# Kernel optimization log

Measured on AMD Instinct MI355X. Metric: run time of the kernel, lower is better.

The kernel has to match this reference:

```python
import jax, jax.numpy as jnp
import numpy as np

IN_F = 4096
OUT_F = 4096
Q_RANK = 2
R_RANK = 2
SCALE = 1.0
B, S = 2, 2048


def setup_inputs() -> dict:
    key = jax.random.key(0)
    ks = jax.random.split(key, 8)
    inp = jax.random.normal(ks[0], (B, S, IN_F), jnp.float32)
    # Q, R come from a QR decomposition of linear.weight.t(); random stand-ins with
    # matching shapes and O(1) scale are fine for a numerical baseline.
    Q = jax.random.normal(ks[1], (IN_F, OUT_F), jnp.float32) / np.sqrt(IN_F).astype(np.float32)
    R = jax.random.normal(ks[2], (OUT_F, OUT_F), jnp.float32) / np.sqrt(OUT_F).astype(np.float32)
    # kron_Q1/Q2 are initialized to identity in __init__ (never re-initialized);
    # add small noise so the rotation path is non-trivial.
    sq1 = IN_F // Q_RANK
    kron_Q1 = jnp.eye(sq1, dtype=jnp.float32) + 0.01 * jax.random.normal(ks[3], (sq1, sq1), jnp.float32)
    kron_Q2 = jnp.eye(Q_RANK, dtype=jnp.float32) + 0.01 * jax.random.normal(ks[4], (Q_RANK, Q_RANK), jnp.float32)
    # kron_R1/R2 use normal init with std = 1/size.
    sr1 = OUT_F // R_RANK
    kron_R1 = jax.random.normal(ks[5], (sr1, sr1), jnp.float32) / sr1
    kron_R2 = jax.random.normal(ks[6], (R_RANK, R_RANK), jnp.float32) / R_RANK
    # lambda_matrix inits to zeros; use small noise so the delta term is exercised.
    lambda_matrix = 0.01 * jax.random.normal(ks[7], (OUT_F,), jnp.float32)
    return {"input": inp, "Q": Q, "R": R, "kron_Q1": kron_Q1, "kron_Q2": kron_Q2,
            "kron_R1": kron_R1, "kron_R2": kron_R2, "lambda_matrix": lambda_matrix}


def reference(input, Q, R, kron_Q1, kron_Q2, kron_R1, kron_R2, lambda_matrix):
    rotation = jnp.kron(kron_Q1, kron_Q2)          # [in, in]
    orth = jnp.kron(kron_R1, kron_R2)              # [out, out]
    # orth @ diag(lambda) @ orth.T without materializing diag
    R_eff = R + (orth * lambda_matrix[None, :]) @ orth.T  # [out, out]
    W_t = rotation @ (Q @ R_eff)                   # [in, out]
    # F.linear(input, W_t.t()) == input @ W_t; dropout is identity in eval; bias=False
    return (input @ W_t) * SCALE
```

## Files before the change

kernel.cpp:

```cpp
#include <hip/hip_runtime.h>
#include <stdint.h>


typedef unsigned short u16;
typedef short bf16x8 __attribute__((ext_vector_type(8)));
typedef float f32x4 __attribute__((ext_vector_type(4)));

__device__ __forceinline__ u16 f2bf(float f) {
  union { float f; uint32_t u; } v; v.f = f;
  return (u16)((v.u + 0x7FFFu + ((v.u >> 16) & 1u)) >> 16);
}

__device__ __forceinline__ void store_out(float* p, float v) { *p = v; }
__device__ __forceinline__ void store_out(u16* p, float v) { *p = f2bf(v); }

__device__ __forceinline__ void gload_lds16(const u16* g, u16* l) {
  __builtin_amdgcn_global_load_lds(
      (__attribute__((address_space(1))) void*)(uintptr_t)g,
      (__attribute__((address_space(3))) void*)l, 16, 0, 0);
}

template <typename OutT>
__global__ __launch_bounds__(512, 2) void gemm256(
    const u16* __restrict__ A, const u16* __restrict__ Bt, OutT* __restrict__ C,
    int M, int N, int K, int ldC, long long sA, long long sC) {
  extern __shared__ __align__(16) u16 smem[];
  u16* ldsA = smem;
  u16* ldsB = smem + 32768;

  const int tid  = (int)threadIdx.x;
  const int lane = tid & 63;
  const int wid  = tid >> 6;
  const int wr   = wid >> 2;
  const int wc   = wid & 3;

  const int tilesX = (int)gridDim.x;
  const int tilesXY = tilesX * (int)gridDim.y;
  const int nwg = tilesXY * (int)gridDim.z;
  const int bid = ((int)blockIdx.z * (int)gridDim.y + (int)blockIdx.y) * tilesX + (int)blockIdx.x;
  const int swz = (bid & 7) * (nwg >> 3) + (bid >> 3);
  const int z   = swz / tilesXY;
  const int rem = swz % tilesXY;
  const int brow = (rem / tilesX) << 8;
  const int bcol = (rem % tilesX) << 8;
  A += (size_t)z * sA;
  C += (size_t)z * sC;

  const int lr = lane & 15, lg = lane >> 4, h = lr >> 1;
  const int sf = (lg + ((lr & 1) << 2)) ^ h;
  const int aoff = (wr * 64 + h) * 64 + sf * 8;
  const int boff = (wc * 32 + h) * 64 + sf * 8;

  const int kp   = (tid & 7) ^ ((tid >> 3) & 7);
  const int srow = 2 * (tid >> 3) + (kp >> 2);
  const int scol = (kp & 3) << 3;
  const size_t gA0 = (size_t)(brow + srow) * K + scol;
  const size_t gA1 = (size_t)(brow + 128 + srow) * K + scol;
  const size_t gB0 = (size_t)(bcol + srow) * K + scol;
  const size_t gB1 = (size_t)(bcol + 128 + srow) * K + scol;
  const int sOff0 = wid * 512;
  const int sOff1 = 4096 + wid * 512;

  const int NC = K >> 5;

  f32x4 acc[8][4] = {};

#define STAGE_A(cc) do { const int _s = ((cc) & 3) * 8192; const size_t _k = (size_t)(cc) * 32; \
    gload_lds16(A + gA0 + _k, ldsA + _s + sOff0);                                               \
    gload_lds16(A + gA1 + _k, ldsA + _s + sOff1); } while (0)
#define STAGE_B(cc) do { const int _s = ((cc) & 3) * 8192; const size_t _k = (size_t)(cc) * 32; \
    gload_lds16(Bt + gB0 + _k, ldsB + _s + sOff0);                                              \
    gload_lds16(Bt + gB1 + _k, ldsB + _s + sOff1); } while (0)

  STAGE_A(0); STAGE_B(0); STAGE_A(1); STAGE_B(1); STAGE_A(2); STAGE_B(2);
  asm volatile("s_waitcnt vmcnt(8)" ::: "memory");
  __builtin_amdgcn_sched_barrier(0);
  __builtin_amdgcn_s_barrier();

#define CHUNK(c, DOSTAGE, TAILWAIT) do {                                        \
    const int _sl = ((c) & 3) * 8192;                                           \
    const u16* _pa = ldsA + _sl + aoff;                                         \
    const u16* _pb = ldsB + _sl + boff;                                         \
    bf16x8 aA[4], aB[4], bb[4];                                                 \
    _Pragma("unroll")                                                           \
    for (int m = 0; m < 4; ++m) aA[m] = *(const bf16x8*)(_pa + m * 512);        \
    _Pragma("unroll")                                                           \
    for (int n = 0; n < 4; ++n) bb[n] = *(const bf16x8*)(_pb + n * 512);        \
    if (DOSTAGE) STAGE_A((c) + 3);                                              \
    __builtin_amdgcn_s_barrier();                                               \
    asm volatile("s_waitcnt lgkmcnt(0)" ::: "memory");                          \
    __builtin_amdgcn_sched_barrier(0);                                          \
    __builtin_amdgcn_s_setprio(1);                                              \
    _Pragma("unroll")                                                           \
    for (int m = 0; m < 4; ++m)                                                 \
      _Pragma("unroll")                                                         \
      for (int n = 0; n < 4; ++n)                                               \
        acc[m][n] = __builtin_amdgcn_mfma_f32_16x16x32_bf16(aA[m], bb[n], acc[m][n], 0, 0, 0); \
    __builtin_amdgcn_s_setprio(0);                                              \
    __builtin_amdgcn_s_barrier();                                               \
    _Pragma("unroll")                                                           \
    for (int m = 0; m < 4; ++m) aB[m] = *(const bf16x8*)(_pa + (4 + m) * 512);  \
    if (DOSTAGE) STAGE_B((c) + 3);                                              \
    __builtin_amdgcn_s_barrier();                                               \
    asm volatile("s_waitcnt lgkmcnt(0)" ::: "memory");                          \
    __builtin_amdgcn_sched_barrier(0);                                          \
    __builtin_amdgcn_s_setprio(1);                                              \
    _Pragma("unroll")                                                           \
    for (int m = 0; m < 4; ++m)                                                 \
      _Pragma("unroll")                                                         \
      for (int n = 0; n < 4; ++n)                                               \
        acc[4 + m][n] = __builtin_amdgcn_mfma_f32_16x16x32_bf16(aB[m], bb[n], acc[4 + m][n], 0, 0, 0); \
    __builtin_amdgcn_s_setprio(0);                                              \
    asm volatile("s_waitcnt " TAILWAIT ::: "memory");                           \
    __builtin_amdgcn_sched_barrier(0);                                          \
    __builtin_amdgcn_s_barrier();                                               \
  } while (0)

  for (int c = 0; c + 3 < NC; ++c) CHUNK(c, 1, "vmcnt(8)");
  CHUNK(NC - 3, 0, "vmcnt(4)");
  CHUNK(NC - 2, 0, "vmcnt(0)");
  CHUNK(NC - 1, 0, "vmcnt(0)");

#undef CHUNK
#undef STAGE_A
#undef STAGE_B

#pragma unroll
  for (int m = 0; m < 8; ++m) {
    const int r0 = brow + wr * 128 + m * 16 + lg * 4;
#pragma unroll
    for (int n = 0; n < 4; ++n) {
      const int cc = bcol + wc * 64 + n * 16 + lr;
#pragma unroll
      for (int j = 0; j < 4; ++j)
        store_out(&C[(size_t)(r0 + j) * ldC + cc], acc[m][n][j]);
    }
  }
}

__global__ void trans_kernel(const float* __restrict__ in, u16* __restrict__ out, int n) {
  __shared__ float t[32][33];
  const int bx = (int)blockIdx.x * 32, by = (int)blockIdx.y * 32;
  const int x = (int)threadIdx.x, y0 = (int)threadIdx.y;
#pragma unroll
  for (int dy = 0; dy < 32; dy += 8)
    t[y0 + dy][x] = in[(size_t)(bx + y0 + dy) * n + by + x];
  __syncthreads();
#pragma unroll
  for (int dy = 0; dy < 32; dy += 8)
    out[(size_t)(by + y0 + dy) * n + bx + x] = f2bf(t[x][y0 + dy]);
}

__global__ void transperm_kernel(const float* __restrict__ in, u16* __restrict__ out) {
  __shared__ float t[32][33];
  const int bx = (int)blockIdx.x * 32, by = (int)blockIdx.y * 32;
  const int x = (int)threadIdx.x, y0 = (int)threadIdx.y;
#pragma unroll
  for (int dy = 0; dy < 32; dy += 8)
    t[y0 + dy][x] = in[(size_t)(bx + y0 + dy) * 4096 + by + x];
  __syncthreads();
  const int r = bx + x;
  const int cp = ((r & 1) << 11) | (r >> 1);
#pragma unroll
  for (int dy = 0; dy < 32; dy += 8)
    out[(size_t)(by + y0 + dy) * 4096 + cp] = f2bf(t[x][y0 + dy]);
}

__global__ void transadd_kernel(const float* __restrict__ R, const float* __restrict__ Dsub,
                                u16* __restrict__ out) {
  __shared__ float t[32][33];
  const int bx = (int)blockIdx.x * 32, by = (int)blockIdx.y * 32;
  const int x = (int)threadIdx.x, y0 = (int)threadIdx.y;
#pragma unroll
  for (int dy = 0; dy < 32; dy += 8)
    t[y0 + dy][x] = R[(size_t)(bx + y0 + dy) * 4096 + by + x];
  __syncthreads();
  const int j = bx + x;
#pragma unroll
  for (int dy = 0; dy < 32; dy += 8) {
    const int i = by + y0 + dy;
    const int s = ((i & 1) << 1) | (j & 1);
    const float d = Dsub[(size_t)s * 4194304 + ((size_t)(i >> 1) << 11) + (j >> 1)];
    out[(size_t)i * 4096 + j] = f2bf(t[x][y0 + dy] + d);
  }
}

__global__ void scale_r1_kernel(const float* __restrict__ R1, const float* __restrict__ R2,
                                const float* __restrict__ lam,
                                u16* __restrict__ R1bf, u16* __restrict__ Asc) {
  const int idx = (int)blockIdx.x * 256 + (int)threadIdx.x;
  const int i1 = idx >> 9, k1 = (idx & 511) << 2;
  const float4 r1 = *(const float4*)(R1 + (size_t)i1 * 2048 + k1);
  const float4 l0 = *(const float4*)(lam + 2 * k1);
  const float4 l1 = *(const float4*)(lam + 2 * k1 + 4);
  const float le[4] = {l0.x, l0.z, l1.x, l1.z};
  const float lo[4] = {l0.y, l0.w, l1.y, l1.w};
  const float rv[4] = {r1.x, r1.y, r1.z, r1.w};
  ushort4 rb;
  rb.x = f2bf(r1.x); rb.y = f2bf(r1.y); rb.z = f2bf(r1.z); rb.w = f2bf(r1.w);
  *(ushort4*)(R1bf + (size_t)i1 * 2048 + k1) = rb;
#pragma unroll
  for (int s = 0; s < 4; ++s) {
    const int i2 = s >> 1, j2 = s & 1;
    const float c0 = R2[i2 * 2] * R2[j2 * 2];
    const float c1 = R2[i2 * 2 + 1] * R2[j2 * 2 + 1];
    ushort4 o;
    u16* dst = Asc + (size_t)s * 4194304 + (size_t)i1 * 2048 + k1;
    o.x = f2bf(rv[0] * (le[0] * c0 + lo[0] * c1));
    o.y = f2bf(rv[1] * (le[1] * c0 + lo[1] * c1));
    o.z = f2bf(rv[2] * (le[2] * c0 + lo[2] * c1));
    o.w = f2bf(rv[3] * (le[3] * c0 + lo[3] * c1));
    *(ushort4*)dst = o;
  }
}

__global__ void tprep_kernel(const float* __restrict__ in, const float* __restrict__ Q2,
                             u16* __restrict__ T) {
  const int idx = (int)blockIdx.x * 256 + (int)threadIdx.x;
  const int s = idx >> 9, k1 = (idx & 511) << 2;
  const float4 a = *(const float4*)(in + (size_t)s * 4096 + 2 * k1);
  const float4 b = *(const float4*)(in + (size_t)s * 4096 + 2 * k1 + 4);
  const float e[4] = {a.x, a.z, b.x, b.z};
  const float o[4] = {a.y, a.w, b.y, b.w};
  const float q00 = Q2[0], q01 = Q2[1], q10 = Q2[2], q11 = Q2[3];
  ushort4 t0, t1;
  t0.x = f2bf(e[0] * q00 + o[0] * q10); t1.x = f2bf(e[0] * q01 + o[0] * q11);
  t0.y = f2bf(e[1] * q00 + o[1] * q10); t1.y = f2bf(e[1] * q01 + o[1] * q11);
  t0.z = f2bf(e[2] * q00 + o[2] * q10); t1.z = f2bf(e[2] * q01 + o[2] * q11);
  t0.w = f2bf(e[3] * q00 + o[3] * q10); t1.w = f2bf(e[3] * q01 + o[3] * q11);
  *(ushort4*)(T + (size_t)s * 2048 + k1) = t0;
  *(ushort4*)(T + 8388608 + (size_t)s * 2048 + k1) = t1;
}

extern "C" void kernel_launch(void* const* d_in, const int* in_sizes, int n_in,
                              void* d_out, int out_size, void* d_ws, size_t ws_size,
                              hipStream_t stream) {
  const float* input = (const float*)d_in[0];
  const float* Q     = (const float*)d_in[1];
  const float* R     = (const float*)d_in[2];
  const float* Q1    = (const float*)d_in[3];
  const float* Q2    = (const float*)d_in[4];
  const float* R1    = (const float*)d_in[5];
  const float* R2    = (const float*)d_in[6];
  const float* lam   = (const float*)d_in[7];
  float* out = (float*)d_out;

  const size_t MB = 1024ull * 1024ull;
  char* ws = (char*)d_ws;
  u16* R1bf  = (u16*)(ws + 0 * MB);
  u16* Asc   = (u16*)(ws + 8 * MB);
  u16* Q1tb  = (u16*)(ws + 40 * MB);
  u16* T     = (u16*)(ws + 48 * MB);
  u16* Qtp   = (u16*)(ws + 80 * MB);
  u16* rteff = (u16*)(ws + 112 * MB);
  u16* X1p   = (u16*)(ws + 144 * MB);
  u16* X2    = Asc;
  float* Dsub = (float*)d_out;

  {
    void (*pf)(const u16*, const u16*, float*, int, int, int, int, long long, long long) = gemm256<float>;
    void (*pb)(const u16*, const u16*, u16*, int, int, int, int, long long, long long)   = gemm256<u16>;
    (void)hipFuncSetAttribute((const void*)pf, hipFuncAttributeMaxDynamicSharedMemorySize, 131072);
    (void)hipFuncSetAttribute((const void*)pb, hipFuncAttributeMaxDynamicSharedMemorySize, 131072);
  }

  const dim3 tb(32, 8);
  trans_kernel<<<dim3(64, 64), tb, 0, stream>>>(Q1, Q1tb, 2048);
  transperm_kernel<<<dim3(128, 128), tb, 0, stream>>>(Q, Qtp);
  scale_r1_kernel<<<4096, 256, 0, stream>>>(R1, R2, lam, R1bf, Asc);
  tprep_kernel<<<8192, 256, 0, stream>>>(input, Q2, T);
  gemm256<float><<<dim3(8, 8, 4), 512, 131072, stream>>>(
      Asc, R1bf, Dsub, 2048, 2048, 2048, 2048, 4194304LL, 4194304LL);
  transadd_kernel<<<dim3(128, 128), tb, 0, stream>>>(R, Dsub, rteff);
  gemm256<u16><<<dim3(8, 16, 2), 512, 131072, stream>>>(
      T, Q1tb, X1p, 4096, 2048, 2048, 4096, 8388608LL, 2048LL);
  gemm256<u16><<<dim3(16, 16, 1), 512, 131072, stream>>>(
      X1p, Qtp, X2, 4096, 4096, 4096, 4096, 0LL, 0LL);
  gemm256<float><<<dim3(16, 16, 1), 512, 131072, stream>>>(
      X2, rteff, out, 4096, 4096, 4096, 4096, 0LL, 0LL);
}
```

Before: 493.6 us.

## Restructure GEMM main loop to BK=64 double-buffered tiles with 8-phase schedule

Reworks the bf16 GEMM main loop from four-stage BK=32 chunks to double-buffered BK=64 tiles, split into eight compute phases per pair of tiles. Global-to-LDS staging of A and B halves is interleaved with MFMA phases, and each phase reuses fragments held in registers across two k-substeps. The aim is to cut barriers per unit of K and improve overlap of memory loads with matrix math. In exchange it holds more fragment registers and adds a tighter, more fragile vmcnt accounting scheme.

```diff
diff --git a/kernel.cpp b/kernel.cpp
--- a/kernel.cpp
+++ b/kernel.cpp
@@ -19,6 +19,8 @@
       (__attribute__((address_space(1))) void*)(uintptr_t)g,
       (__attribute__((address_space(3))) void*)l, 16, 0, 0);
 }
+
+#define MFMA16(a, b, c) __builtin_amdgcn_mfma_f32_16x16x32_bf16((a), (b), (c), 0, 0, 0)
 
 template <typename OutT>
 __global__ __launch_bounds__(512, 2) void gemm256(
@@ -48,82 +50,100 @@
 
   const int lr = lane & 15, lg = lane >> 4, h = lr >> 1;
   const int sf = (lg + ((lr & 1) << 2)) ^ h;
-  const int aoff = (wr * 64 + h) * 64 + sf * 8;
-  const int boff = (wc * 32 + h) * 64 + sf * 8;
+  const int abase = wr * 8192 + h * 64 + sf * 8;
+  const int bbase = (wc >> 1) * 8192 + ((wc & 1) * 32 + h) * 64 + sf * 8;
 
   const int kp   = (tid & 7) ^ ((tid >> 3) & 7);
   const int srow = 2 * (tid >> 3) + (kp >> 2);
   const int scol = (kp & 3) << 3;
   const size_t gA0 = (size_t)(brow + srow) * K + scol;
-  const size_t gA1 = (size_t)(brow + 128 + srow) * K + scol;
   const size_t gB0 = (size_t)(bcol + srow) * K + scol;
-  const size_t gB1 = (size_t)(bcol + 128 + srow) * K + scol;
-  const int sOff0 = wid * 512;
-  const int sOff1 = 4096 + wid * 512;
-
-  const int NC = K >> 5;
+  const size_t rstep = (size_t)K << 7;
+  const int sdst = wid * 512;
+
+  const int NC = K >> 6;
+  const int NI = NC >> 1;
 
   f32x4 acc[8][4] = {};
-
-#define STAGE_A(cc) do { const int _s = ((cc) & 3) * 8192; const size_t _k = (size_t)(cc) * 32; \
-    gload_lds16(A + gA0 + _k, ldsA + _s + sOff0);                                               \
-    gload_lds16(A + gA1 + _k, ldsA + _s + sOff1); } while (0)
-#define STAGE_B(cc) do { const int _s = ((cc) & 3) * 8192; const size_t _k = (size_t)(cc) * 32; \
-    gload_lds16(Bt + gB0 + _k, ldsB + _s + sOff0);                                              \
-    gload_lds16(Bt + gB1 + _k, ldsB + _s + sOff1); } while (0)
-
-  STAGE_A(0); STAGE_B(0); STAGE_A(1); STAGE_B(1); STAGE_A(2); STAGE_B(2);
-  asm volatile("s_waitcnt vmcnt(8)" ::: "memory");
-  __builtin_amdgcn_sched_barrier(0);
-  __builtin_amdgcn_s_barrier();
-
-#define CHUNK(c, DOSTAGE, TAILWAIT) do {                                        \
-    const int _sl = ((c) & 3) * 8192;                                           \
-    const u16* _pa = ldsA + _sl + aoff;                                         \
-    const u16* _pb = ldsB + _sl + boff;                                         \
-    bf16x8 aA[4], aB[4], bb[4];                                                 \
-    _Pragma("unroll")                                                           \
-    for (int m = 0; m < 4; ++m) aA[m] = *(const bf16x8*)(_pa + m * 512);        \
-    _Pragma("unroll")                                                           \
-    for (int n = 0; n < 4; ++n) bb[n] = *(const bf16x8*)(_pb + n * 512);        \
-    if (DOSTAGE) STAGE_A((c) + 3);                                              \
+  bf16x8 af[4][2], bf[4][2];
+
+#define STG_A(t, rh, ks) gload_lds16(A + gA0 + (rh) * rstep + (size_t)(t) * 64 + (ks) * 32, \
+    ldsA + ((t) & 1) * 16384 + (rh) * 8192 + (ks) * 4096 + sdst)
+#define STG_B(t, rh, ks) gload_lds16(Bt + gB0 + (rh) * rstep + (size_t)(t) * 64 + (ks) * 32, \
+    ldsB + ((t) & 1) * 16384 + (rh) * 8192 + (ks) * 4096 + sdst)
+#define VM4 asm volatile("s_waitcnt vmcnt(4)" ::: "memory")
+#define VM0 asm volatile("s_waitcnt vmcnt(0)" ::: "memory")
+
+#define PH(BUF, MH, RDA, RDB01, RDB23, N0, N1, S0, S1, TAIL) do {               \
+    const u16* _pa = ldsA + (BUF) * 16384 + abase;                              \
+    const u16* _pb = ldsB + (BUF) * 16384 + bbase;                              \
+    if (RDA) {                                                                  \
+      _Pragma("unroll")                                                         \
+      for (int m = 0; m < 4; ++m) {                                             \
+        af[m][0] = *(const bf16x8*)(_pa + ((MH) * 4 + m) * 512);                \
+        af[m][1] = *(const bf16x8*)(_pa + ((MH) * 4 + m) * 512 + 4096);         \
+      }                                                                         \
+    }                                                                           \
+    if (RDB01) {                                                                \
+      bf[0][0] = *(const bf16x8*)(_pb);        bf[0][1] = *(const bf16x8*)(_pb + 4096);       \
+      bf[1][0] = *(const bf16x8*)(_pb + 512);  bf[1][1] = *(const bf16x8*)(_pb + 512 + 4096); \
+    }                                                                           \
+    if (RDB23) {                                                                \
+      bf[2][0] = *(const bf16x8*)(_pb + 1024); bf[2][1] = *(const bf16x8*)(_pb + 1024 + 4096); \
+      bf[3][0] = *(const bf16x8*)(_pb + 1536); bf[3][1] = *(const bf16x8*)(_pb + 1536 + 4096); \
+    }                                                                           \
+    S0; S1;                                                                     \
     __builtin_amdgcn_s_barrier();                                               \
     asm volatile("s_waitcnt lgkmcnt(0)" ::: "memory");                          \
     __builtin_amdgcn_sched_barrier(0);                                          \
     __builtin_amdgcn_s_setprio(1);                                              \
     _Pragma("unroll")                                                           \
-    for (int m = 0; m < 4; ++m)                                                 \
-      _Pragma("unroll")                                                         \
-      for (int n = 0; n < 4; ++n)                                               \
-        acc[m][n] = __builtin_amdgcn_mfma_f32_16x16x32_bf16(aA[m], bb[n], acc[m][n], 0, 0, 0); \
+    for (int m = 0; m < 4; ++m) {                                               \
+      acc[(MH) * 4 + m][N0] = MFMA16(af[m][0], bf[N0][0], acc[(MH) * 4 + m][N0]); \
+      acc[(MH) * 4 + m][N0] = MFMA16(af[m][1], bf[N0][1], acc[(MH) * 4 + m][N0]); \
+      acc[(MH) * 4 + m][N1] = MFMA16(af[m][0], bf[N1][0], acc[(MH) * 4 + m][N1]); \
+      acc[(MH) * 4 + m][N1] = MFMA16(af[m][1], bf[N1][1], acc[(MH) * 4 + m][N1]); \
+    }                                                                           \
     __builtin_amdgcn_s_setprio(0);                                              \
-    __builtin_amdgcn_s_barrier();                                               \
-    _Pragma("unroll")                                                           \
-    for (int m = 0; m < 4; ++m) aB[m] = *(const bf16x8*)(_pa + (4 + m) * 512);  \
-    if (DOSTAGE) STAGE_B((c) + 3);                                              \
-    __builtin_amdgcn_s_barrier();                                               \
-    asm volatile("s_waitcnt lgkmcnt(0)" ::: "memory");                          \
-    __builtin_amdgcn_sched_barrier(0);                                          \
-    __builtin_amdgcn_s_setprio(1);                                              \
-    _Pragma("unroll")                                                           \
-    for (int m = 0; m < 4; ++m)                                                 \
-      _Pragma("unroll")                                                         \
-      for (int n = 0; n < 4; ++n)                                               \
-        acc[4 + m][n] = __builtin_amdgcn_mfma_f32_16x16x32_bf16(aB[m], bb[n], acc[4 + m][n], 0, 0, 0); \
-    __builtin_amdgcn_s_setprio(0);                                              \
-    asm volatile("s_waitcnt " TAILWAIT ::: "memory");                           \
+    TAIL;                                                                       \
     __builtin_amdgcn_sched_barrier(0);                                          \
     __builtin_amdgcn_s_barrier();                                               \
   } while (0)
 
-  for (int c = 0; c + 3 < NC; ++c) CHUNK(c, 1, "vmcnt(8)");
-  CHUNK(NC - 3, 0, "vmcnt(4)");
-  CHUNK(NC - 2, 0, "vmcnt(0)");
-  CHUNK(NC - 1, 0, "vmcnt(0)");
-
-#undef CHUNK
-#undef STAGE_A
-#undef STAGE_B
+  STG_A(0, 0, 0); STG_A(0, 0, 1); STG_A(0, 1, 0); STG_A(0, 1, 1);
+  STG_B(0, 0, 0); STG_B(0, 0, 1); STG_B(0, 1, 0); STG_B(0, 1, 1);
+  STG_B(1, 0, 0); STG_B(1, 0, 1); STG_B(1, 1, 0); STG_B(1, 1, 1);
+  VM4;
+  __builtin_amdgcn_sched_barrier(0);
+  __builtin_amdgcn_s_barrier();
+
+  for (int i = 0; i < NI - 1; ++i) {
+    const int tn = 2 * i;
+    PH(0, 0, 1, 1, 0, 0, 1, STG_A(tn + 1, 0, 0), STG_A(tn + 1, 0, 1), (void)0);
+    PH(0, 0, 0, 0, 1, 2, 3, STG_A(tn + 1, 1, 0), STG_A(tn + 1, 1, 1), (void)0);
+    PH(0, 1, 1, 0, 0, 0, 1, STG_B(tn + 2, 0, 0), STG_B(tn + 2, 0, 1), (void)0);
+    PH(0, 1, 0, 0, 0, 2, 3, STG_B(tn + 2, 1, 0), STG_B(tn + 2, 1, 1), VM4);
+    PH(1, 0, 1, 1, 0, 0, 1, STG_A(tn + 2, 0, 0), STG_A(tn + 2, 0, 1), (void)0);
+    PH(1, 0, 0, 0, 1, 2, 3, STG_A(tn + 2, 1, 0), STG_A(tn + 2, 1, 1), (void)0);
+    PH(1, 1, 1, 0, 0, 0, 1, STG_B(tn + 3, 0, 0), STG_B(tn + 3, 0, 1), (void)0);
+    PH(1, 1, 0, 0, 0, 2, 3, STG_B(tn + 3, 1, 0), STG_B(tn + 3, 1, 1), VM4);
+  }
+  {
+    PH(0, 0, 1, 1, 0, 0, 1, STG_A(NC - 1, 0, 0), STG_A(NC - 1, 0, 1), (void)0);
+    PH(0, 0, 0, 0, 1, 2, 3, STG_A(NC - 1, 1, 0), STG_A(NC - 1, 1, 1), (void)0);
+    PH(0, 1, 1, 0, 0, 0, 1, (void)0, (void)0, (void)0);
+    PH(0, 1, 0, 0, 0, 2, 3, (void)0, (void)0, VM0);
+    PH(1, 0, 1, 1, 0, 0, 1, (void)0, (void)0, (void)0);
+    PH(1, 0, 0, 0, 1, 2, 3, (void)0, (void)0, (void)0);
+    PH(1, 1, 1, 0, 0, 0, 1, (void)0, (void)0, (void)0);
+    PH(1, 1, 0, 0, 0, 2, 3, (void)0, (void)0, (void)0);
+  }
+
+#undef PH
+#undef STG_A
+#undef STG_B
+#undef VM4
+#undef VM0
 
 #pragma unroll
   for (int m = 0; m < 8; ++m) {
```

Measured after the change: 460.4 us. 1.07x faster.
